# Kernel optimization log

Measured on AMD Instinct MI355X. Metric: run time of the kernel, lower is better.

Reference implementation:

```python
import jax, jax.numpy as jnp
from jax import lax
import numpy as np

MSS = 1448.0
MAX_RTT = 0.01
B, S = 2048, 4096


def setup_inputs() -> dict:
    key = jax.random.key(0)
    k1, k2, k3, k4 = jax.random.split(key, 4)
    # packet lengths in [0, 1500) bytes so bursts aggregate past MSS=1448
    x = jax.random.uniform(k1, (B, S), jnp.float32) * 1500.0
    mask = jax.random.uniform(k2, (B, S)) < 0.1
    scale = 0.00094557476340694
    d_exp = 1e-6 + scale * jax.random.exponential(k3, (B, S), jnp.float32)
    delays = jnp.where(mask, jnp.float32(0.21), d_exp)
    # per-burst RTT samples, indexed by the burst-start packet position
    rtts = jax.random.uniform(k4, (B, S), jnp.float32) * MAX_RTT
    return {"x": x, "delays": delays, "rtts": rtts}


def _simulate_row(x, delays, rtts):
    # x, delays, rtts: [S]
    S_ = x.shape[0]

    def step(carry, inp):
        active, new_burst, r = carry
        xj, dj, rj = inp
        # outer-while check only at burst start: stop forever if x[j] <= 0
        active = jnp.where(new_burst, active & (xj > 0), active)
        r = jnp.where(new_burst, rj, r)
        r_next = r - dj  # inner while: RTT -= delays[j]
        burst_end = active & (r_next <= 0)
        start_flag = new_burst & active
        return (active, burst_end, r_next), (active, start_flag)

    init = (jnp.bool_(True), jnp.bool_(True), jnp.float32(0.0))
    _, (consumed, start_flag) = lax.scan(step, init, (x, delays, rtts))

    # per-burst buffered byte count: segment-sum of consumed packet lengths
    burst_id = jnp.clip(jnp.cumsum(start_flag.astype(jnp.int32)) - 1, 0, S_ - 1)
    buf = jax.ops.segment_sum(jnp.where(consumed, x, 0.0), burst_id, num_segments=S_)

    # `while buf > MSS` emits ceil(buf/MSS)-1 full segments, then remainder
    n_full = jnp.maximum(jnp.ceil(buf / MSS).astype(jnp.int32) - 1, 0)
    rem = buf - n_full.astype(x.dtype) * MSS
    has_rem = rem > 0
    count = n_full + has_rem.astype(jnp.int32)
    starts = jnp.cumsum(count) - count  # exclusive cumsum: output offset per burst
    ends = starts + n_full

    # difference-array trick: positions in [starts, ends) get MSS (OOB drops == truncation)
    diff = (jnp.zeros(S_, jnp.int32)
            .at[starts].add(1, mode='drop')
            .at[ends].add(-1, mode='drop'))
    cover = jnp.cumsum(diff) > 0
    out = jnp.where(cover, jnp.float32(MSS), jnp.float32(0.0))

    # remainder goes right after the MSS run of its burst
    rem_pos = jnp.where(has_rem, ends, S_)  # S_ -> dropped
    out = out.at[rem_pos].set(rem, mode='drop')
    return out


def reference(x, delays, rtts):
    out = jax.vmap(_simulate_row)(x, delays, rtts)  # [B, S]
    return out[..., None]  # unsqueeze(-1) -> [B, S, 1]
```

## Files before the change

kernel.cpp:

```cpp
#include <hip/hip_runtime.h>
#include <math.h>


#define S_LEN 4096
#define BLOCK 512
#define PER   8
#define MSSF  1448.0f
#define ATHR  0.01f

#define OFF_NXT   0
#define OFF_MARK  16384
#define OFF_DEATH 20480
#define OFF_WS    20496
#define SMEM_SZ   20528

#define EXT(K) ((K) < 16 ? dla[(K)] : dlb[(K) - 16])

__global__ __launch_bounds__(BLOCK, 6) void traffic_kernel(
    const float* __restrict__ gx,
    const float* __restrict__ gd,
    const float* __restrict__ gr,
    float* __restrict__ gout)
{
    __shared__ __align__(16) unsigned char smem[SMEM_SZ];
    unsigned short* s_nxt  = (unsigned short*)(smem + OFF_NXT);
    int*            s_diff = (int*)(smem + OFF_NXT);
    float*          s_out  = (float*)(smem + OFF_NXT);
    unsigned char*  s_mark = (unsigned char*)(smem + OFF_MARK);
    int*            s_death= (int*)(smem + OFF_DEATH);
    int*            s_ws   = (int*)(smem + OFF_WS);

    const int tid = threadIdx.x;
    const int sb  = tid << 3;
    const size_t rowoff = (size_t)blockIdx.x * S_LEN;
    const float* px = gx + rowoff;
    const float* pd = gd + rowoff;
    const float* pr = gr + rowoff;

    float xreg[PER];
    float rt[PER];
    {
        float4 xa = *(const float4*)(px + sb);
        float4 xb = *(const float4*)(px + sb + 4);
        xreg[0]=xa.x; xreg[1]=xa.y; xreg[2]=xa.z; xreg[3]=xa.w;
        xreg[4]=xb.x; xreg[5]=xb.y; xreg[6]=xb.z; xreg[7]=xb.w;
        float4 ra = *(const float4*)(pr + sb);
        float4 rb = *(const float4*)(pr + sb + 4);
        rt[0]=ra.x; rt[1]=ra.y; rt[2]=ra.z; rt[3]=ra.w;
        rt[4]=rb.x; rt[5]=rb.y; rt[6]=rb.z; rt[7]=rb.w;
    }
    float dla[16], dlb[8];
    if (sb + 16 <= S_LEN) {
        const float4* dv = (const float4*)(pd + sb);
        float4 a0 = dv[0], a1 = dv[1], a2 = dv[2], a3 = dv[3];
        dla[0]=a0.x;  dla[1]=a0.y;  dla[2]=a0.z;  dla[3]=a0.w;
        dla[4]=a1.x;  dla[5]=a1.y;  dla[6]=a1.z;  dla[7]=a1.w;
        dla[8]=a2.x;  dla[9]=a2.y;  dla[10]=a2.z; dla[11]=a2.w;
        dla[12]=a3.x; dla[13]=a3.y; dla[14]=a3.z; dla[15]=a3.w;
    } else {
#pragma unroll
        for (int q = 0; q < 16; ++q)
            dla[q] = (sb + q < S_LEN) ? pd[sb + q] : 1.0e30f;
    }
    if (sb + 24 <= S_LEN) {
        const float4* dv = (const float4*)(pd + sb + 16);
        float4 b0 = dv[0], b1 = dv[1];
        dlb[0]=b0.x; dlb[1]=b0.y; dlb[2]=b0.z; dlb[3]=b0.w;
        dlb[4]=b1.x; dlb[5]=b1.y; dlb[6]=b1.z; dlb[7]=b1.w;
    } else {
#pragma unroll
        for (int q = 0; q < 8; ++q)
            dlb[q] = (sb + 16 + q < S_LEN) ? pd[sb + 16 + q] : 1.0e30f;
    }
    float dm1 = (tid == 0) ? 1.0e30f : pd[sb - 1];

    unsigned amask = (dm1 >= ATHR) ? 1u : 0u;
#pragma unroll
    for (int k = 1; k <= 24; ++k)
        amask |= (EXT(k - 1) >= ATHR) ? (1u << k) : 0u;

    unsigned surv = 0;
    float rsv[PER];
    int nx8[PER];
#pragma unroll
    for (int i = 0; i < PER; ++i) {
        float r1 = rt[i] - dla[i];
        float r2 = r1 - dla[i + 1];
        float r3 = r2 - dla[i + 2];
        float r4 = r3 - dla[i + 3];
        float r5 = r4 - dla[i + 4];
        float r6 = r5 - dla[i + 5];
        float r7 = r6 - dla[i + 6];
        float r8 = r7 - dla[i + 7];
        int c = (r1 > 0.0f) + (r2 > 0.0f) + (r3 > 0.0f) + (r4 > 0.0f) +
                (r5 > 0.0f) + (r6 > 0.0f) + (r7 > 0.0f) + (r8 > 0.0f);
        rsv[i] = r8;
        int nx = sb + i + c + 1;
        if (nx > S_LEN) nx = S_LEN;
        nx8[i] = nx;
        if (c == 8) surv |= 1u << i;
    }

    unsigned surv2 = 0;
    if (surv) {
#pragma unroll
        for (int i = 0; i < PER; ++i) {
            if ((surv >> i) & 1u) {
                float rr = rsv[i];
                float q1 = rr - EXT(i + 8);
                float q2 = q1 - EXT(i + 9);
                float q3 = q2 - EXT(i + 10);
                float q4 = q3 - EXT(i + 11);
                float q5 = q4 - EXT(i + 12);
                float q6 = q5 - EXT(i + 13);
                float q7 = q6 - EXT(i + 14);
                float q8 = q7 - EXT(i + 15);
                int c2 = (q1 > 0.0f) + (q2 > 0.0f) + (q3 > 0.0f) + (q4 > 0.0f) +
                         (q5 > 0.0f) + (q6 > 0.0f) + (q7 > 0.0f) + (q8 > 0.0f);
                rsv[i] = q8;
                if (c2 == 8) {
                    surv2 |= 1u << i;
                } else {
                    int nx = sb + i + 8 + c2 + 1;
                    if (nx > S_LEN) nx = S_LEN;
                    nx8[i] = nx;
                }
            }
        }
    }

    while (surv2) {
        int i = __ffs(surv2) - 1;
        surv2 &= surv2 - 1;
        float rr = rsv[0];
#pragma unroll
        for (int ii = 1; ii < PER; ++ii) rr = (i == ii) ? rsv[ii] : rr;
        int j = sb + i + 16;
        int nx;
        while (true) {
            float e0 = 1.0e30f, e1 = 1.0e30f, e2 = 1.0e30f, e3 = 1.0e30f;
            float e4 = 1.0e30f, e5 = 1.0e30f, e6 = 1.0e30f, e7 = 1.0e30f;
            if (j     < S_LEN) e0 = pd[j];
            if (j + 1 < S_LEN) e1 = pd[j + 1];
            if (j + 2 < S_LEN) e2 = pd[j + 2];
            if (j + 3 < S_LEN) e3 = pd[j + 3];
            if (j + 4 < S_LEN) e4 = pd[j + 4];
            if (j + 5 < S_LEN) e5 = pd[j + 5];
            if (j + 6 < S_LEN) e6 = pd[j + 6];
            if (j + 7 < S_LEN) e7 = pd[j + 7];
            float q1 = rr - e0;
            float q2 = q1 - e1;
            float q3 = q2 - e2;
            float q4 = q3 - e3;
            float q5 = q4 - e4;
            float q6 = q5 - e5;
            float q7 = q6 - e6;
            float q8 = q7 - e7;
            int c2 = (q1 > 0.0f) + (q2 > 0.0f) + (q3 > 0.0f) + (q4 > 0.0f) +
                     (q5 > 0.0f) + (q6 > 0.0f) + (q7 > 0.0f) + (q8 > 0.0f);
            if (c2 < 8) { nx = j + c2 + 1; break; }
            j += 8;
            rr = q8;
        }
        if (nx > S_LEN) nx = S_LEN;
#pragma unroll
        for (int ii = 0; ii < PER; ++ii) nx8[ii] = (ii == i) ? nx : nx8[ii];
    }

    {
        int enc[PER];
#pragma unroll
        for (int i = 0; i < PER; ++i) {
            int v = nx8[i];
            int e;
            if (!(xreg[i] > 0.0f)) {
                e = 0xFFFF;
            } else if (v >= S_LEN) {
                e = S_LEN;
            } else {
                int rel = v - sb;
                int flag = (rel <= 24) ? (int)((amask >> rel) & 1u)
                                       : ((pd[v - 1] >= ATHR) ? 1 : 0);
                e = v | (flag << 15);
            }
            enc[i] = e;
        }
        uint4 pk;
        pk.x = (unsigned)enc[0] | ((unsigned)enc[1] << 16);
        pk.y = (unsigned)enc[2] | ((unsigned)enc[3] << 16);
        pk.z = (unsigned)enc[4] | ((unsigned)enc[5] << 16);
        pk.w = (unsigned)enc[6] | ((unsigned)enc[7] << 16);
        *(uint4*)&s_nxt[sb] = pk;
    }
    *(unsigned long long*)(s_mark + sb) = 0ull;
    if (tid == 0) *s_death = 0x7FFFFFFF;
    __syncthreads();

    {
        unsigned a8 = amask & 0xFFu;
        while (a8) {
            int i = __ffs(a8) - 1;
            a8 &= a8 - 1;
            int p = sb + i;
            while (true) {
                int v = (int)s_nxt[p];
                if (v == 0xFFFF) { atomicMin(s_death, p); break; }
                s_mark[p] = 1;
                if (v & 0x8000) break;
                if (v >= S_LEN) break;
                p = v;
            }
        }
    }
    __syncthreads();

    unsigned lm;
    {
        unsigned long long mv = *(const unsigned long long*)(s_mark + sb);
        unsigned m0 = (unsigned)mv, m1 = (unsigned)(mv >> 32);
        lm = (((m0 & 0x01010101u) * 0x01020408u) >> 24)
           | ((((m1 & 0x01010101u) * 0x01020408u) >> 24) << 4);
        int dp = *s_death;
        if (dp < S_LEN) {
            if (sb > dp) lm = 0;
            else if (sb + 7 > dp) lm &= (1u << (dp - sb + 1)) - 1u;
        }
    }

    float xnxt[8];
    if (sb + 16 <= S_LEN) {
        float4 a = *(const float4*)(px + sb + 8);
        float4 b = *(const float4*)(px + sb + 12);
        xnxt[0]=a.x; xnxt[1]=a.y; xnxt[2]=a.z; xnxt[3]=a.w;
        xnxt[4]=b.x; xnxt[5]=b.y; xnxt[6]=b.z; xnxt[7]=b.w;
    } else {
#pragma unroll
        for (int q = 0; q < 8; ++q)
            xnxt[q] = (sb + 8 + q < S_LEN) ? px[sb + 8 + q] : 0.0f;
    }
    int      nfF[9];
    float    remF[9];
    unsigned fl = 0;
    int      tsum = 0;
    {
        float cs = 0.0f;
        int   ce = 0;
        bool  open = false;
#pragma unroll
        for (int i = 0; i < PER; ++i) {
            if ((lm >> i) & 1u) {
                if (open) {
                    int nf = (int)ceilf(cs / MSSF) - 1; if (nf < 0) nf = 0;
                    float rem = cs - (float)nf * MSSF;
                    nfF[i] = nf; remF[i] = rem;
                    fl |= 1u << i;
                    tsum += nf + (rem > 0.0f ? 1 : 0);
                }
                open = true; cs = 0.0f; ce = nx8[i];
            }
            cs += (open && (sb + i < ce)) ? xreg[i] : 0.0f;
        }
        if (open) {
            int upper = ce - sb;
#pragma unroll
            for (int q = 0; q < 8; ++q)
                cs += (q + 8 < upper) ? xnxt[q] : 0.0f;
            int j = sb + 16;
            for (; j + 8 <= ce; j += 8) {
                float4 a = *(const float4*)(px + j);
                float4 b = *(const float4*)(px + j + 4);
                cs += a.x; cs += a.y; cs += a.z; cs += a.w;
                cs += b.x; cs += b.y; cs += b.z; cs += b.w;
            }
            for (; j < ce; ++j) cs += px[j];
            int nf = (int)ceilf(cs / MSSF) - 1; if (nf < 0) nf = 0;
            float rem = cs - (float)nf * MSSF;
            nfF[8] = nf; remF[8] = rem;
            fl |= 1u << 8;
            tsum += nf + (rem > 0.0f ? 1 : 0);
        }
    }

    {
        int4* d4 = (int4*)s_diff;
        int4 z; z.x = z.y = z.z = z.w = 0;
        d4[tid] = z;
        d4[tid + 512] = z;
    }
    int texcl;
    {
        int lane = tid & 63, wv = tid >> 6;
        int v = tsum;
        for (int off = 1; off < 64; off <<= 1) {
            int u = __shfl_up(v, off, 64);
            if (lane >= off) v += u;
        }
        if (lane == 63) s_ws[wv] = v;
        __syncthreads();
        int4 w0 = *(const int4*)s_ws;
        int4 w1 = *(const int4*)(s_ws + 4);
        int woff = 0;
        woff += (wv > 0) ? w0.x : 0;
        woff += (wv > 1) ? w0.y : 0;
        woff += (wv > 2) ? w0.z : 0;
        woff += (wv > 3) ? w0.w : 0;
        woff += (wv > 4) ? w1.x : 0;
        woff += (wv > 5) ? w1.y : 0;
        woff += (wv > 6) ? w1.z : 0;
        texcl = woff + v - tsum;
    }

    {
        int o = texcl;
#pragma unroll
        for (int i = 0; i < 9; ++i) {
            if ((fl >> i) & 1u) {
                int nf = nfF[i];
                if (nf > 0) {
                    if (o < S_LEN) atomicAdd(&s_diff[o], 1);
                    int e2 = o + nf;
                    if (e2 < S_LEN) atomicAdd(&s_diff[e2], -1);
                }
                o += nf + (remF[i] > 0.0f ? 1 : 0);
            }
        }
    }
    __syncthreads();

    {
        int4 a = *(int4*)&s_diff[sb];
        int4 b = *(int4*)&s_diff[sb + 4];
        int v0 = a.x,      v1 = v0 + a.y, v2 = v1 + a.z, v3 = v2 + a.w;
        int v4 = v3 + b.x, v5 = v4 + b.y, v6 = v5 + b.z, v7 = v6 + b.w;
        int T = v7;
        int lane = tid & 63, wv = tid >> 6;
        int sc = T;
        for (int off = 1; off < 64; off <<= 1) {
            int u = __shfl_up(sc, off, 64);
            if (lane >= off) sc += u;
        }
        if (lane == 63) s_ws[wv] = sc;
        __syncthreads();
        int4 w0 = *(const int4*)s_ws;
        int4 w1 = *(const int4*)(s_ws + 4);
        int basev = 0;
        basev += (wv > 0) ? w0.x : 0;
        basev += (wv > 1) ? w0.y : 0;
        basev += (wv > 2) ? w0.z : 0;
        basev += (wv > 3) ? w0.w : 0;
        basev += (wv > 4) ? w1.x : 0;
        basev += (wv > 5) ? w1.y : 0;
        basev += (wv > 6) ? w1.z : 0;
        basev += sc - T;
        float4 fa, fb;
        fa.x = (basev + v0 > 0) ? MSSF : 0.0f;
        fa.y = (basev + v1 > 0) ? MSSF : 0.0f;
        fa.z = (basev + v2 > 0) ? MSSF : 0.0f;
        fa.w = (basev + v3 > 0) ? MSSF : 0.0f;
        fb.x = (basev + v4 > 0) ? MSSF : 0.0f;
        fb.y = (basev + v5 > 0) ? MSSF : 0.0f;
        fb.z = (basev + v6 > 0) ? MSSF : 0.0f;
        fb.w = (basev + v7 > 0) ? MSSF : 0.0f;
        *(float4*)&s_out[sb]     = fa;
        *(float4*)&s_out[sb + 4] = fb;
    }
    __syncthreads();

    {
        int o = texcl;
#pragma unroll
        for (int i = 0; i < 9; ++i) {
            if ((fl >> i) & 1u) {
                int nf = nfF[i];
                float rem = remF[i];
                int rp = o + nf;
                if (rem > 0.0f && rp < S_LEN) s_out[rp] = rem;
                o += nf + (rem > 0.0f ? 1 : 0);
            }
        }
    }
    __syncthreads();

    {
        float4* po4 = (float4*)(gout + rowoff);
        const float4* so4 = (const float4*)s_out;
        po4[tid]       = so4[tid];
        po4[tid + 512] = so4[tid + 512];
    }
}

extern "C" void kernel_launch(void* const* d_in, const int* in_sizes, int n_in,
                              void* d_out, int out_size, void* d_ws, size_t ws_size,
                              hipStream_t stream) {
    const float* x      = (const float*)d_in[0];
    const float* delays = (const float*)d_in[1];
    const float* rtts   = (const float*)d_in[2];
    float* out = (float*)d_out;
    int rows = in_sizes[0] / S_LEN;
    traffic_kernel<<<rows, BLOCK, 0, stream>>>(x, delays, rtts, out);
}
```

Measured before the change: 158.2 us.

## Write remainders to separate smem buffer and store output directly to global

```diff
diff --git a/kernel.cpp b/kernel.cpp
--- a/kernel.cpp
+++ b/kernel.cpp
@@ -10,9 +10,10 @@
 
 #define OFF_NXT   0
 #define OFF_MARK  16384
-#define OFF_DEATH 20480
-#define OFF_WS    20496
-#define SMEM_SZ   20528
+#define OFF_REM   20480
+#define OFF_DEATH 36864
+#define OFF_WS    36880
+#define SMEM_SZ   36912
 
 #define EXT(K) ((K) < 16 ? dla[(K)] : dlb[(K) - 16])
 
@@ -25,8 +26,8 @@
     __shared__ __align__(16) unsigned char smem[SMEM_SZ];
     unsigned short* s_nxt  = (unsigned short*)(smem + OFF_NXT);
     int*            s_diff = (int*)(smem + OFF_NXT);
-    float*          s_out  = (float*)(smem + OFF_NXT);
     unsigned char*  s_mark = (unsigned char*)(smem + OFF_MARK);
+    float*          s_rem  = (float*)(smem + OFF_REM);
     int*            s_death= (int*)(smem + OFF_DEATH);
     int*            s_ws   = (int*)(smem + OFF_WS);
 
@@ -79,54 +80,23 @@
     for (int k = 1; k <= 24; ++k)
         amask |= (EXT(k - 1) >= ATHR) ? (1u << k) : 0u;
 
-    unsigned surv = 0;
+    unsigned surv2 = 0;
     float rsv[PER];
     int nx8[PER];
 #pragma unroll
     for (int i = 0; i < PER; ++i) {
-        float r1 = rt[i] - dla[i];
-        float r2 = r1 - dla[i + 1];
-        float r3 = r2 - dla[i + 2];
-        float r4 = r3 - dla[i + 3];
-        float r5 = r4 - dla[i + 4];
-        float r6 = r5 - dla[i + 5];
-        float r7 = r6 - dla[i + 6];
-        float r8 = r7 - dla[i + 7];
-        int c = (r1 > 0.0f) + (r2 > 0.0f) + (r3 > 0.0f) + (r4 > 0.0f) +
-                (r5 > 0.0f) + (r6 > 0.0f) + (r7 > 0.0f) + (r8 > 0.0f);
-        rsv[i] = r8;
+        float r = rt[i];
+        int c = 0;
+#pragma unroll
+        for (int k = 0; k < 16; ++k) {
+            r = r - EXT(i + k);
+            c += (r > 0.0f) ? 1 : 0;
+        }
+        rsv[i] = r;
         int nx = sb + i + c + 1;
         if (nx > S_LEN) nx = S_LEN;
         nx8[i] = nx;
-        if (c == 8) surv |= 1u << i;
-    }
-
-    unsigned surv2 = 0;
-    if (surv) {
-#pragma unroll
-        for (int i = 0; i < PER; ++i) {
-            if ((surv >> i) & 1u) {
-                float rr = rsv[i];
-                float q1 = rr - EXT(i + 8);
-                float q2 = q1 - EXT(i + 9);
-                float q3 = q2 - EXT(i + 10);
-                float q4 = q3 - EXT(i + 11);
-                float q5 = q4 - EXT(i + 12);
-                float q6 = q5 - EXT(i + 13);
-                float q7 = q6 - EXT(i + 14);
-                float q8 = q7 - EXT(i + 15);
-                int c2 = (q1 > 0.0f) + (q2 > 0.0f) + (q3 > 0.0f) + (q4 > 0.0f) +
-                         (q5 > 0.0f) + (q6 > 0.0f) + (q7 > 0.0f) + (q8 > 0.0f);
-                rsv[i] = q8;
-                if (c2 == 8) {
-                    surv2 |= 1u << i;
-                } else {
-                    int nx = sb + i + 8 + c2 + 1;
-                    if (nx > S_LEN) nx = S_LEN;
-                    nx8[i] = nx;
-                }
-            }
-        }
+        if (c == 16) surv2 |= 1u << i;
     }
 
     while (surv2) {
@@ -286,6 +256,10 @@
         int4 z; z.x = z.y = z.z = z.w = 0;
         d4[tid] = z;
         d4[tid + 512] = z;
+        float4* r4 = (float4*)s_rem;
+        float4 zf; zf.x = zf.y = zf.z = zf.w = 0.0f;
+        r4[tid] = zf;
+        r4[tid + 512] = zf;
     }
     int texcl;
     {
@@ -321,7 +295,14 @@
                     int e2 = o + nf;
                     if (e2 < S_LEN) atomicAdd(&s_diff[e2], -1);
                 }
-                o += nf + (remF[i] > 0.0f ? 1 : 0);
+                float rem = remF[i];
+                if (rem > 0.0f) {
+                    int rp = o + nf;
+                    if (rp < S_LEN) s_rem[rp] = rem;
+                    o += nf + 1;
+                } else {
+                    o += nf;
+                }
             }
         }
     }
@@ -352,40 +333,19 @@
         basev += (wv > 5) ? w1.y : 0;
         basev += (wv > 6) ? w1.z : 0;
         basev += sc - T;
+        float4 ra4 = *(const float4*)&s_rem[sb];
+        float4 rb4 = *(const float4*)&s_rem[sb + 4];
         float4 fa, fb;
-        fa.x = (basev + v0 > 0) ? MSSF : 0.0f;
-        fa.y = (basev + v1 > 0) ? MSSF : 0.0f;
-        fa.z = (basev + v2 > 0) ? MSSF : 0.0f;
-        fa.w = (basev + v3 > 0) ? MSSF : 0.0f;
-        fb.x = (basev + v4 > 0) ? MSSF : 0.0f;
-        fb.y = (basev + v5 > 0) ? MSSF : 0.0f;
-        fb.z = (basev + v6 > 0) ? MSSF : 0.0f;
-        fb.w = (basev + v7 > 0) ? MSSF : 0.0f;
-        *(float4*)&s_out[sb]     = fa;
-        *(float4*)&s_out[sb + 4] = fb;
-    }
-    __syncthreads();
-
-    {
-        int o = texcl;
-#pragma unroll
-        for (int i = 0; i < 9; ++i) {
-            if ((fl >> i) & 1u) {
-                int nf = nfF[i];
-                float rem = remF[i];
-                int rp = o + nf;
-                if (rem > 0.0f && rp < S_LEN) s_out[rp] = rem;
-                o += nf + (rem > 0.0f ? 1 : 0);
-            }
-        }
-    }
-    __syncthreads();
-
-    {
-        float4* po4 = (float4*)(gout + rowoff);
-        const float4* so4 = (const float4*)s_out;
-        po4[tid]       = so4[tid];
-        po4[tid + 512] = so4[tid + 512];
+        fa.x = (basev + v0 > 0) ? MSSF : ra4.x;
+        fa.y = (basev + v1 > 0) ? MSSF : ra4.y;
+        fa.z = (basev + v2 > 0) ? MSSF : ra4.z;
+        fa.w = (basev + v3 > 0) ? MSSF : ra4.w;
+        fb.x = (basev + v4 > 0) ? MSSF : rb4.x;
+        fb.y = (basev + v5 > 0) ? MSSF : rb4.y;
+        fb.z = (basev + v6 > 0) ? MSSF : rb4.z;
+        fb.w = (basev + v7 > 0) ? MSSF : rb4.w;
+        *(float4*)(gout + rowoff + sb)     = fa;
+        *(float4*)(gout + rowoff + sb + 4) = fb;
     }
 }
 
```

Result: no change. 157.4 us (-0.5%).
